# Kernel optimization log

Hardware: AMD Instinct MI355X
Metric: run time of the kernel (lower is better)

The kernel has to match this reference:

```python
import jax, jax.numpy as jnp
import numpy as np

WINDOW_SIZE = 11
N_CHANNELS = 3
SIGMA = 1.5
K1, K2 = 0.01, 0.03
VALUE_RANGE = 1.0


def _create_window(window_size: int, n_channels: int, sigma: float) -> np.ndarray:
    # 1D gaussian, normalized, then outer product -> 2D kernel
    coords = np.arange(window_size, dtype=np.float32) - (window_size - 1) / 2.0
    g = np.exp(-(coords ** 2) / (2.0 * sigma ** 2))
    g = g / g.sum()
    k2d = np.outer(g, g).astype(np.float32)  # (K, K), sums to 1
    # depthwise kernel, OIHW with I=1 (groups = n_channels)
    return np.broadcast_to(k2d, (n_channels, 1, window_size, window_size)).copy()


def _dwconv(x, window):
    # depthwise valid conv, NCHW / OIHW
    return jax.lax.conv_general_dilated(
        x, window, window_strides=(1, 1), padding='VALID',
        feature_group_count=window.shape[0],
        dimension_numbers=('NCHW', 'OIHW', 'NCHW'))


def setup_inputs() -> dict:
    key = jax.random.key(0)
    kx, ky = jax.random.split(key)
    N, C, H, W = 32, N_CHANNELS, 512, 512
    x = jax.random.uniform(kx, (N, C, H, W), dtype=jnp.float32)
    y = jax.random.uniform(ky, (N, C, H, W), dtype=jnp.float32)
    window = jnp.asarray(_create_window(WINDOW_SIZE, N_CHANNELS, SIGMA))
    return {"x": x, "y": y, "window": window}


def reference(x, y, window):
    c1 = (K1 * VALUE_RANGE) ** 2
    c2 = (K2 * VALUE_RANGE) ** 2

    mu_x = _dwconv(x, window)
    mu_y = _dwconv(y, window)
    mu_x_sq = mu_x ** 2
    mu_y_sq = mu_y ** 2
    mu_xy = mu_x * mu_y

    sigma_x_sq = _dwconv(x * x, window) - mu_x_sq
    sigma_y_sq = _dwconv(y * y, window) - mu_y_sq
    sigma_xy = _dwconv(x * y, window) - mu_xy

    cs = (2.0 * sigma_xy + c2) / (sigma_x_sq + sigma_y_sq + c2)
    ss = (2.0 * mu_xy + c1) / (mu_x_sq + mu_y_sq + c1) * cs

    l = ss.mean(axis=(-1, -2))  # (N, C) per-channel SSIM
    l = l.mean(axis=-1)         # (N,)  per-sample
    return l.mean()             # reduction='mean'
```

## Files before the change

kernel.cpp:

```cpp
#include <hip/hip_runtime.h>

typedef float v2f __attribute__((ext_vector_type(2)));

#define KS    11
#define HH    512
#define WW    512
#define OUTD  502
#define OH    34
#define ROWS  44
#define NBR   15
#define NBC   2
#define TC    256
#define SG    266
#define NIMG  96

__global__ __launch_bounds__(256, 3)
void ssim_main(const float* __restrict__ xg, const float* __restrict__ yg,
               const float* __restrict__ win, double* __restrict__ acc_out)
{
    __shared__ v2f buf[2][SG];
    __shared__ float wsums[4];

    const int tid = threadIdx.x;
    int bb = blockIdx.x;
    const int img   = bb % NIMG;  bb /= NIMG;
    const int band  = bb % NBR;   bb /= NBR;
    const int ctile = bb;
    const int row0  = band * OH;
    const int cb    = ctile * TC;

    float g[KS];
    #pragma unroll
    for (int i = 0; i < KS; i++) {
        float s = 0.f;
        #pragma unroll
        for (int j = 0; j < KS; j++) s += win[i * KS + j];
        g[i] = s;
    }

    const float* xi = xg + (size_t)img * HH * WW;
    const float* yi = yg + (size_t)img * HH * WW;

    v2f   aMu[KS], aSq[KS];
    float aXy[KS];
    #pragma unroll
    for (int s = 0; s < KS; s++) {
        aMu[s] = (v2f)0.f; aSq[s] = (v2f)0.f; aXy[s] = 0.f;
    }

    float ssum = 0.f;
    const float C1 = 0.0001f;
    const float C2 = 0.0009f;

    float px0, py0, px1, py1;
    auto load_row = [&](int r, float& x0, float& y0, float& x1, float& y1) {
        int gr = row0 + r; if (gr > HH - 1) gr = HH - 1;
        const size_t base = (size_t)gr * WW;
        const int gc0 = cb + tid;
        x0 = xi[base + gc0]; y0 = yi[base + gc0];
        x1 = 0.f; y1 = 0.f;
        if (tid < SG - TC) {
            const int gc1 = cb + TC + tid;
            if (gc1 < WW) { x1 = xi[base + gc1]; y1 = yi[base + gc1]; }
        }
    };
    auto store_row = [&](int bsel, float x0, float y0, float x1, float y1) {
        v2f v; v.x = x0; v.y = y0;
        buf[bsel][tid] = v;
        if (tid < SG - TC) { v2f w; w.x = x1; w.y = y1; buf[bsel][TC + tid] = w; }
    };

    load_row(0, px0, py0, px1, py1);
    store_row(0, px0, py0, px1, py1);
    load_row(1, px0, py0, px1, py1);
    __syncthreads();

    #pragma unroll 1
    for (int rb = 0; rb < ROWS / KS; rb++) {
        #pragma unroll
        for (int rr = 0; rr < KS; rr++) {
            const int r = rb * KS + rr;
            const v2f* bufr = buf[r & 1];

            if (r + 1 < ROWS) store_row((r + 1) & 1, px0, py0, px1, py1);
            if (r + 2 < ROWS) load_row(r + 2, px0, py0, px1, py1);

            v2f hMu = (v2f)0.f, hSq = (v2f)0.f;
            float hXy = 0.f;
            #pragma unroll
            for (int j = 0; j < KS; j++) {
                const v2f v = bufr[tid + j];
                v2f gg; gg.x = g[j]; gg.y = g[j];
                hMu = __builtin_elementwise_fma(gg, v, hMu);
                const v2f sq = v * v;
                hSq = __builtin_elementwise_fma(gg, sq, hSq);
                hXy = fmaf(g[j], v.x * v.y, hXy);
            }

            #pragma unroll
            for (int i = 0; i < KS; i++) {
                const int slot = (rr - i + KS) % KS;
                v2f gg; gg.x = g[i]; gg.y = g[i];
                aMu[slot] = __builtin_elementwise_fma(gg, hMu, aMu[slot]);
                aSq[slot] = __builtin_elementwise_fma(gg, hSq, aSq[slot]);
                aXy[slot] = fmaf(g[i], hXy, aXy[slot]);
            }

            const int es   = (rr + 1) % KS;
            const int jloc = r - (KS - 1);
            if (jloc >= 0 && (row0 + jloc) < OUTD && (cb + tid) < OUTD) {
                const float mx  = aMu[es].x, my  = aMu[es].y;
                const float Sxx = aSq[es].x, Syy = aSq[es].y, Sxy = aXy[es];
                const float mxx = mx * mx, myy = my * my, mxy = mx * my;
                const float sxx = Sxx - mxx, syy = Syy - myy, sxy = Sxy - mxy;
                const float num = (2.f * mxy + C1) * (2.f * sxy + C2);
                const float den = (mxx + myy + C1) * (sxx + syy + C2);
                float rc = __builtin_amdgcn_rcpf(den);
                rc = rc * fmaf(-den, rc, 2.0f);
                ssum = fmaf(num, rc, ssum);
            }
            aMu[es] = (v2f)0.f; aSq[es] = (v2f)0.f; aXy[es] = 0.f;

            __syncthreads();
        }
    }

    #pragma unroll
    for (int off = 32; off > 0; off >>= 1)
        ssum += __shfl_down(ssum, off);
    const int wave = tid >> 6;
    if ((tid & 63) == 0) wsums[wave] = ssum;
    __syncthreads();
    if (tid == 0) {
        float s = wsums[0] + wsums[1] + wsums[2] + wsums[3];
        atomicAdd(acc_out, (double)s);
    }
}

__global__ void ssim_finalize(const double* __restrict__ acc, float* __restrict__ out)
{
    out[0] = (float)(acc[0] * (1.0 / 24192384.0));
}

extern "C" void kernel_launch(void* const* d_in, const int* in_sizes, int n_in,
                              void* d_out, int out_size, void* d_ws, size_t ws_size,
                              hipStream_t stream)
{
    const float* x   = (const float*)d_in[0];
    const float* y   = (const float*)d_in[1];
    const float* win = (const float*)d_in[2];
    float* out = (float*)d_out;
    double* acc = (double*)d_ws;

    hipMemsetAsync(acc, 0, sizeof(double), stream);
    ssim_main<<<dim3(NIMG * NBR * NBC), dim3(256), 0, stream>>>(x, y, win, acc);
    ssim_finalize<<<dim3(1), dim3(1), 0, stream>>>(acc, out);
}
```

Measured before the change: 293.2 us.

## Stage 11-row groups in LDS with float4 loads and packed FMA asm

Replaces the per-row double-buffered staging with 11-row groups loaded via float4 vector loads, interleaved into x/y pairs, and prefetched two groups ahead. Barriers drop from one per row to two per group. Inline v_pk_fma/v_pk_mul asm is used, and the symmetric Gaussian taps are stored as 6 packed values to save registers. The larger LDS buffer (about 23KB) and extra prefetch registers may reduce occupancy, and a single buffer forces a barrier before each store.

```diff
diff --git a/kernel.cpp b/kernel.cpp
--- a/kernel.cpp
+++ b/kernel.cpp
@@ -7,108 +7,124 @@
 #define WW    512
 #define OUTD  502
 #define OH    34
-#define ROWS  44
+#define GR    11
+#define NG    4
 #define NBR   15
 #define NBC   2
 #define TC    256
-#define SG    266
+#define CH    67
+#define SGL   268
 #define NIMG  96
+#define ITEMS (GR * CH)
+
+__device__ __forceinline__ v2f pk_fma(v2f a, v2f b, v2f c) {
+    v2f d;
+    asm("v_pk_fma_f32 %0, %1, %2, %3" : "=v"(d) : "v"(a), "v"(b), "v"(c));
+    return d;
+}
+__device__ __forceinline__ v2f pk_mul(v2f a, v2f b) {
+    v2f d;
+    asm("v_pk_mul_f32 %0, %1, %2" : "=v"(d) : "v"(a), "v"(b));
+    return d;
+}
 
 __global__ __launch_bounds__(256, 3)
 void ssim_main(const float* __restrict__ xg, const float* __restrict__ yg,
                const float* __restrict__ win, double* __restrict__ acc_out)
 {
-    __shared__ v2f buf[2][SG];
+    __shared__ v2f buf[GR][SGL];
     __shared__ float wsums[4];
 
     const int tid = threadIdx.x;
     int bb = blockIdx.x;
-    const int img   = bb % NIMG;  bb /= NIMG;
-    const int band  = bb % NBR;   bb /= NBR;
-    const int ctile = bb;
-    const int row0  = band * OH;
-    const int cb    = ctile * TC;
+    const int img  = bb % NIMG;  bb /= NIMG;
+    const int band = bb % NBR;   bb /= NBR;
+    const int cb   = bb * TC;
+    const int row0 = band * OH;
 
-    float g[KS];
+    v2f g2[6];
     #pragma unroll
-    for (int i = 0; i < KS; i++) {
+    for (int i = 0; i < 6; i++) {
         float s = 0.f;
         #pragma unroll
         for (int j = 0; j < KS; j++) s += win[i * KS + j];
-        g[i] = s;
+        v2f p; p.x = s; p.y = s; g2[i] = p;
     }
 
-    const float* xi = xg + (size_t)img * HH * WW;
-    const float* yi = yg + (size_t)img * HH * WW;
+    const float* xi = xg + (size_t)img * (HH * WW);
+    const float* yi = yg + (size_t)img * (HH * WW);
 
-    v2f   aMu[KS], aSq[KS];
-    float aXy[KS];
+    float4 pfx[3], pfy[3];
+    auto prefetch = [&](int g) {
+        #pragma unroll
+        for (int it = 0; it < 3; it++) {
+            const int idx = tid + 256 * it;
+            if (it < 2 || idx < ITEMS) {
+                int i = idx / CH, k = idx - i * CH;
+                int gr = row0 + g * GR + i; if (gr > HH - 1) gr = HH - 1;
+                int gc = cb + 4 * k;        if (gc > WW - 4) gc = WW - 4;
+                const size_t base = (size_t)gr * WW + gc;
+                pfx[it] = *(const float4*)(xi + base);
+                pfy[it] = *(const float4*)(yi + base);
+            }
+        }
+    };
+    auto store_s = [&]() {
+        #pragma unroll
+        for (int it = 0; it < 3; it++) {
+            const int idx = tid + 256 * it;
+            if (it < 2 || idx < ITEMS) {
+                int i = idx / CH, k = idx - i * CH;
+                const float4 xv = pfx[it], yv = pfy[it];
+                float4 a; a.x = xv.x; a.y = yv.x; a.z = xv.y; a.w = yv.y;
+                float4 b; b.x = xv.z; b.y = yv.z; b.z = xv.w; b.w = yv.w;
+                *(float4*)&buf[i][4 * k]     = a;
+                *(float4*)&buf[i][4 * k + 2] = b;
+            }
+        }
+    };
+
+    v2f aMu[KS], aSq[KS]; float aXy[KS];
     #pragma unroll
-    for (int s = 0; s < KS; s++) {
-        aMu[s] = (v2f)0.f; aSq[s] = (v2f)0.f; aXy[s] = 0.f;
-    }
+    for (int s = 0; s < KS; s++) { aMu[s] = (v2f)0.f; aSq[s] = (v2f)0.f; aXy[s] = 0.f; }
 
     float ssum = 0.f;
     const float C1 = 0.0001f;
     const float C2 = 0.0009f;
+    const bool colvalid = (cb + tid) < OUTD;
 
-    float px0, py0, px1, py1;
-    auto load_row = [&](int r, float& x0, float& y0, float& x1, float& y1) {
-        int gr = row0 + r; if (gr > HH - 1) gr = HH - 1;
-        const size_t base = (size_t)gr * WW;
-        const int gc0 = cb + tid;
-        x0 = xi[base + gc0]; y0 = yi[base + gc0];
-        x1 = 0.f; y1 = 0.f;
-        if (tid < SG - TC) {
-            const int gc1 = cb + TC + tid;
-            if (gc1 < WW) { x1 = xi[base + gc1]; y1 = yi[base + gc1]; }
-        }
-    };
-    auto store_row = [&](int bsel, float x0, float y0, float x1, float y1) {
-        v2f v; v.x = x0; v.y = y0;
-        buf[bsel][tid] = v;
-        if (tid < SG - TC) { v2f w; w.x = x1; w.y = y1; buf[bsel][TC + tid] = w; }
-    };
-
-    load_row(0, px0, py0, px1, py1);
-    store_row(0, px0, py0, px1, py1);
-    load_row(1, px0, py0, px1, py1);
+    prefetch(0); store_s(); prefetch(1);
     __syncthreads();
 
     #pragma unroll 1
-    for (int rb = 0; rb < ROWS / KS; rb++) {
+    for (int g = 0; g < NG; g++) {
         #pragma unroll
-        for (int rr = 0; rr < KS; rr++) {
-            const int r = rb * KS + rr;
-            const v2f* bufr = buf[r & 1];
+        for (int rr = 0; rr < GR; rr++) {
+            const v2f* rowp = &buf[rr][tid];
 
-            if (r + 1 < ROWS) store_row((r + 1) & 1, px0, py0, px1, py1);
-            if (r + 2 < ROWS) load_row(r + 2, px0, py0, px1, py1);
-
-            v2f hMu = (v2f)0.f, hSq = (v2f)0.f;
-            float hXy = 0.f;
+            v2f hMu = (v2f)0.f, hSq = (v2f)0.f; float hXy = 0.f;
             #pragma unroll
             for (int j = 0; j < KS; j++) {
-                const v2f v = bufr[tid + j];
-                v2f gg; gg.x = g[j]; gg.y = g[j];
-                hMu = __builtin_elementwise_fma(gg, v, hMu);
-                const v2f sq = v * v;
-                hSq = __builtin_elementwise_fma(gg, sq, hSq);
-                hXy = fmaf(g[j], v.x * v.y, hXy);
+                const v2f gj = g2[j < 6 ? j : 10 - j];
+                const v2f v = rowp[j];
+                hMu = pk_fma(gj, v, hMu);
+                hSq = pk_fma(gj, pk_mul(v, v), hSq);
+                hXy = fmaf(gj.x, v.x * v.y, hXy);
             }
 
             #pragma unroll
             for (int i = 0; i < KS; i++) {
                 const int slot = (rr - i + KS) % KS;
-                v2f gg; gg.x = g[i]; gg.y = g[i];
-                aMu[slot] = __builtin_elementwise_fma(gg, hMu, aMu[slot]);
-                aSq[slot] = __builtin_elementwise_fma(gg, hSq, aSq[slot]);
-                aXy[slot] = fmaf(g[i], hXy, aXy[slot]);
+                const v2f gi = g2[i < 6 ? i : 10 - i];
+                aMu[slot] = pk_fma(gi, hMu, aMu[slot]);
+                aSq[slot] = pk_fma(gi, hSq, aSq[slot]);
+                aXy[slot] = fmaf(gi.x, hXy, aXy[slot]);
             }
 
             const int es   = (rr + 1) % KS;
+            const int r    = g * GR + rr;
             const int jloc = r - (KS - 1);
-            if (jloc >= 0 && (row0 + jloc) < OUTD && (cb + tid) < OUTD) {
+            if (jloc >= 0 && (row0 + jloc) < OUTD && colvalid) {
                 const float mx  = aMu[es].x, my  = aMu[es].y;
                 const float Sxx = aSq[es].x, Syy = aSq[es].y, Sxy = aXy[es];
                 const float mxx = mx * mx, myy = my * my, mxy = mx * my;
@@ -120,8 +136,13 @@
                 ssum = fmaf(num, rc, ssum);
             }
             aMu[es] = (v2f)0.f; aSq[es] = (v2f)0.f; aXy[es] = 0.f;
+        }
 
+        __syncthreads();
+        if (g < NG - 1) {
+            store_s();
             __syncthreads();
+            if (g < NG - 2) prefetch(g + 2);
         }
     }
 
```

Result: faster. 285.2 us (-2.7%).
